# Performance work log

Hardware: AMD Instinct MI355X
Metric: run time of the kernel (lower is better)

## Reference

```python
import jax, jax.numpy as jnp
import numpy as np

# SamplesLoss('sinkhorn', p=2, blur=0.05, backend='tensorized') defaults (geomloss):
# debiased Sinkhorn divergence, cost C(x,y)=|x-y|^2/2, eps = blur^p,
# epsilon-scaling from diameter^p down to blur^p with scaling=0.5,
# symmetric (averaged) log-domain updates + one final extrapolation step.
P = 2
BLUR = 0.05
SCALING = 0.5
DIAMETER = 10.0  # static diameter estimate for the annealing schedule (randn data)


def _eps_schedule():
    eps_target = BLUR ** P
    lst = []
    e = DIAMETER ** P
    while e > eps_target:
        lst.append(e)
        e *= SCALING ** P
    lst.append(eps_target)
    return lst

EPS_LIST = _eps_schedule()


def _sqcost(x, y):
    # C[b,n,m] = 0.5 * ||x_bn - y_bm||^2, via expansion (avoids [B,N,M,D] tensor)
    x2 = jnp.sum(x * x, axis=-1)  # [B,N]
    y2 = jnp.sum(y * y, axis=-1)  # [B,M]
    xy = jnp.einsum('bnd,bmd->bnm', x, y)
    return 0.5 * (x2[:, :, None] + y2[:, None, :] - 2.0 * xy)


def _softmin(eps, C, h):
    # h: [B,M] (already log-weights + potential/eps); C: [B,N,M] -> [B,N]
    return -eps * jax.nn.logsumexp(h[:, None, :] - C / eps, axis=2)


def _sinkhorn_divergence(x, y, a, b):
    log_a = jnp.log(a)
    log_b = jnp.log(b)
    Cxy = _sqcost(x, y)
    Cyx = jnp.swapaxes(Cxy, 1, 2)
    Cxx = _sqcost(x, x)
    Cyy = _sqcost(y, y)

    eps0 = EPS_LIST[0]
    f_ba = _softmin(eps0, Cxy, log_b)  # potential on x for OT(a,b)
    g_ab = _softmin(eps0, Cyx, log_a)  # potential on y for OT(a,b)
    f_aa = _softmin(eps0, Cxx, log_a)  # debias self-potential on x
    g_bb = _softmin(eps0, Cyy, log_b)  # debias self-potential on y

    for eps in EPS_LIST:
        ft = _softmin(eps, Cxy, log_b + g_ab / eps)
        gt = _softmin(eps, Cyx, log_a + f_ba / eps)
        f_ba = 0.5 * (f_ba + ft)
        g_ab = 0.5 * (g_ab + gt)
        f_aa = 0.5 * (f_aa + _softmin(eps, Cxx, log_a + f_aa / eps))
        g_bb = 0.5 * (g_bb + _softmin(eps, Cyy, log_b + g_bb / eps))

    # final (non-averaged) extrapolation at the target temperature
    eps = EPS_LIST[-1]
    f_fin = _softmin(eps, Cxy, log_b + g_ab / eps)
    g_fin = _softmin(eps, Cyx, log_a + f_ba / eps)
    f_aa = _softmin(eps, Cxx, log_a + f_aa / eps)
    g_bb = _softmin(eps, Cyy, log_b + g_bb / eps)

    # debiased divergence: <a, f_ab - f_aa> + <b, g_ab - g_bb>
    return jnp.sum(a * (f_fin - f_aa), axis=-1) + jnp.sum(b * (g_fin - g_bb), axis=-1)


def setup_inputs() -> dict:
    key = jax.random.key(0)
    k1, k2, k3, k4 = jax.random.split(key, 4)
    B, N, M, D = 8, 2048, 2048, 64
    return {
        'inp1': jax.random.normal(k1, (B, N, D), dtype=jnp.float32),
        'inp2': jax.random.normal(k2, (B, M, D), dtype=jnp.float32),
        'weights1': jax.random.uniform(k3, (B, N), dtype=jnp.float32),
        'weights2': jax.random.uniform(k4, (B, M), dtype=jnp.float32),
    }


def reference(inp1, inp2, weights1, weights2):
    # normalize_weights=True branch of SinkhornLoss.forward
    mass1 = jnp.sum(weights1, axis=1, keepdims=True)
    mass1 = jnp.where(mass1 == 0.0, 1.0, mass1)
    a = weights1 / mass1
    mass2 = jnp.sum(weights2, axis=1, keepdims=True)
    mass2 = jnp.where(mass2 == 0.0, 1.0, mass2)
    b = weights2 / mass2
    loss = _sinkhorn_divergence(inp1, inp2, a, b)  # [B]
    return jnp.mean(loss)  # reduction='mean'
```

## Files before the change

### kernel.cpp

```cpp
#include <hip/hip_runtime.h>
#include <cstdint>
#include <cstddef>

#define BB 8
#define NPTS 2048
#define DIM 64
#define CK 64
#define NC (NPTS / CK)
#define BROWS 64

typedef _Float16 f16x8 __attribute__((ext_vector_type(8)));
typedef float f32x4 __attribute__((ext_vector_type(4)));

static const float EPS_H[9] = {100.0f, 25.0f, 6.25f, 1.5625f, 0.390625f,
                               0.09765625f, 0.0244140625f, 0.006103515625f,
                               0.0025f};

#if __has_builtin(__builtin_amdgcn_exp2f)
static __device__ __forceinline__ float fexp2(float x) {
  return __builtin_amdgcn_exp2f(x);
}
#else
static __device__ __forceinline__ float fexp2(float x) {
  float r;
  asm("v_exp_f32 %0, %1" : "=v"(r) : "v"(x));
  return r;
}
#endif

static __device__ __forceinline__ f32x4 vmax4(f32x4 a, f32x4 b) {
  f32x4 r;
  #pragma unroll
  for (int i = 0; i < 4; ++i) r[i] = fmaxf(a[i], b[i]);
  return r;
}

static __device__ __forceinline__ f32x4 vexp2_4(f32x4 a) {
  f32x4 r;
  #pragma unroll
  for (int i = 0; i < 4; ++i) r[i] = fexp2(a[i]);
  return r;
}

static __device__ __forceinline__ void gload_lds16(const void* g, void* l) {
  __builtin_amdgcn_global_load_lds(
      (const __attribute__((address_space(1))) void*)g,
      (__attribute__((address_space(3))) void*)l, 16, 0, 0);
}

struct SMTask {
  const _Float16* P;
  const _Float16* Q;
  const float* logw;
  const float* pot;
  const float* qsq;
  const float* psq;
  const float* oldf;
  float* out;
};


__global__ __launch_bounds__(256) void norm_weights_k(
    const float* __restrict__ w, float* __restrict__ aout,
    float* __restrict__ logout, int n) {
  int b = blockIdx.x;
  const float* wb = w + (size_t)b * n;
  __shared__ float red[256];
  float s = 0.f;
  for (int i = threadIdx.x; i < n; i += 256) s += wb[i];
  red[threadIdx.x] = s;
  __syncthreads();
  for (int st = 128; st > 0; st >>= 1) {
    if (threadIdx.x < st) red[threadIdx.x] += red[threadIdx.x + st];
    __syncthreads();
  }
  float mass = red[0];
  if (mass == 0.f) mass = 1.f;
  float inv = 1.f / mass;
  for (int i = threadIdx.x; i < n; i += 256) {
    float av = wb[i] * inv;
    aout[(size_t)b * n + i] = av;
    logout[(size_t)b * n + i] = logf(av);
  }
}

__global__ __launch_bounds__(256) void sqnorm_cvt_k(
    const float* __restrict__ X, float* __restrict__ sq,
    _Float16* __restrict__ Xh, int rows) {
  int row = blockIdx.x * 4 + (threadIdx.x >> 6);
  int lane = threadIdx.x & 63;
  if (row >= rows) return;
  float v = X[(size_t)row * DIM + lane];
  Xh[(size_t)row * DIM + lane] = (_Float16)v;
  float s = v * v;
  #pragma unroll
  for (int off = 32; off > 0; off >>= 1) s += __shfl_xor(s, off);
  if (lane == 0) sq[row] = s;
}

__global__ __launch_bounds__(256, 4) void fused_softmin_k(
    SMTask t0, SMTask t1, SMTask t2, SMTask t3, float ie2, float neg_eps_ln2) {
  __shared__ float hq[NPTS];
  __shared__ __align__(16) _Float16 qb[2][CK * DIM];
  SMTask T = (blockIdx.z == 0) ? t0
           : (blockIdx.z == 1) ? t1
           : (blockIdx.z == 2) ? t2 : t3;
  const int b = blockIdx.y;
  const int tid = threadIdx.x;
  const float LOG2E = 1.4426950408889634f;
  {
    const float* lw = T.logw + (size_t)b * NPTS;
    const float* q2 = T.qsq + (size_t)b * NPTS;
    const float* pt = T.pot ? T.pot + (size_t)b * NPTS : nullptr;
    for (int m = tid; m < NPTS; m += 256) {
      float h = fmaf(lw[m], LOG2E, -0.5f * q2[m] * ie2);
      if (pt) h = fmaf(pt[m], ie2, h);
      hq[m] = h;
    }
  }

  const int lane = tid & 63, wave = tid >> 6;
  const _Float16* Qb = T.Q + (size_t)b * NPTS * DIM;

  auto stage = [&](int buf, int chunk) {
    int m0 = chunk * CK;
    #pragma unroll
    for (int r = 0; r < 2; ++r) {
      int gbase = r * 256 + wave * 64;
      int gid = gbase + lane;
      int row = gid >> 3;
      int kg = (gid & 7) ^ (row & 7);
      const _Float16* src = Qb + (size_t)(m0 + row) * DIM + kg * 8;
      _Float16* dst = &qb[buf][(size_t)gbase * 8];
      gload_lds16(src, dst);
    }
  };

  const int fr = lane & 15;
  const int g0 = lane >> 4;
  const int r0 = blockIdx.x * BROWS + wave * 16;
  const _Float16* Pb = T.P + ((size_t)b * NPTS + r0) * DIM;
  f16x8 a0 = *(const f16x8*)(Pb + fr * DIM + g0 * 8);
  f16x8 a1 = *(const f16x8*)(Pb + fr * DIM + g0 * 8 + 32);

  f32x4 mx4 = {-3.0e38f, -3.0e38f, -3.0e38f, -3.0e38f};
  f32x4 sm4 = {0.f, 0.f, 0.f, 0.f};

  auto compute = [&](int cur, int m0) {
    const char* qbase = (const char*)&qb[cur][0];
    f32x4 v4[4];
    f32x4 cmx = mx4;
    #pragma unroll
    for (int s = 0; s < 4; ++s) {
      int row = s * 16 + fr;
      int byte0 = row * 128 + ((g0 ^ (row & 7)) << 4);
      int byte1 = row * 128 + (((g0 + 4) ^ (row & 7)) << 4);
      f16x8 b0 = *(const f16x8*)(qbase + byte0);
      f16x8 b1 = *(const f16x8*)(qbase + byte1);
      float hs = hq[m0 + s * 16 + fr];
      f32x4 z = {0.f, 0.f, 0.f, 0.f};
      f32x4 t = __builtin_amdgcn_mfma_f32_16x16x32_f16(a0, b0, z, 0, 0, 0);
      f32x4 acc = __builtin_amdgcn_mfma_f32_16x16x32_f16(a1, b1, t, 0, 0, 0);
      v4[s] = acc * ie2 + hs;
      cmx = vmax4(cmx, v4[s]);
    }
    f32x4 resc = vexp2_4(mx4 - cmx);
    f32x4 esum = vexp2_4(v4[0] - cmx) + vexp2_4(v4[1] - cmx);
    esum += vexp2_4(v4[2] - cmx) + vexp2_4(v4[3] - cmx);
    sm4 = sm4 * resc + esum;
    mx4 = cmx;
  };

  stage(0, 0);
  __syncthreads();

  for (int c = 0; c < NC - 1; ++c) {
    int cur = c & 1;
    stage(cur ^ 1, c + 1);
    asm volatile("s_waitcnt vmcnt(2)" ::: "memory");
    __builtin_amdgcn_sched_barrier(0);
    __builtin_amdgcn_s_barrier();
    __builtin_amdgcn_sched_barrier(0);
    compute(cur, c * CK);
    __builtin_amdgcn_sched_barrier(0);
    __builtin_amdgcn_s_barrier();
    __builtin_amdgcn_sched_barrier(0);
  }
  asm volatile("s_waitcnt vmcnt(0)" ::: "memory");
  __builtin_amdgcn_sched_barrier(0);
  __builtin_amdgcn_s_barrier();
  __builtin_amdgcn_sched_barrier(0);
  compute((NC - 1) & 1, (NC - 1) * CK);

  #pragma unroll
  for (int off = 1; off < 16; off <<= 1) {
    #pragma unroll
    for (int q = 0; q < 4; ++q) {
      float omx = __shfl_xor(mx4[q], off);
      float osm = __shfl_xor(sm4[q], off);
      float nm = fmaxf(mx4[q], omx);
      sm4[q] = sm4[q] * fexp2(mx4[q] - nm) + osm * fexp2(omx - nm);
      mx4[q] = nm;
    }
  }
  if (fr == 0) {
    #pragma unroll
    for (int q = 0; q < 4; ++q) {
      int r = r0 + g0 * 4 + q;
      size_t oi = (size_t)b * NPTS + r;
      float f = neg_eps_ln2 * (__log2f(sm4[q]) + mx4[q]) + 0.5f * T.psq[oi];
      if (T.oldf) f = 0.5f * (T.oldf[oi] + f);
      T.out[oi] = f;
    }
  }
}

__global__ __launch_bounds__(256) void loss_part_k(
    const float* __restrict__ aW, const float* __restrict__ f_fin,
    const float* __restrict__ f_aa, const float* __restrict__ bW,
    const float* __restrict__ g_fin, const float* __restrict__ g_bb,
    float* __restrict__ part) {
  __shared__ float red[256];
  int i0 = blockIdx.x * 256 + threadIdx.x;
  float s = 0.f;
  for (int i = i0; i < BB * NPTS; i += 64 * 256)
    s += aW[i] * (f_fin[i] - f_aa[i]) + bW[i] * (g_fin[i] - g_bb[i]);
  red[threadIdx.x] = s;
  __syncthreads();
  for (int st = 128; st > 0; st >>= 1) {
    if (threadIdx.x < st) red[threadIdx.x] += red[threadIdx.x + st];
    __syncthreads();
  }
  if (threadIdx.x == 0) part[blockIdx.x] = red[0];
}

__global__ __launch_bounds__(64) void loss_fin_k(const float* __restrict__ part,
                                                 float* __restrict__ out) {
  float s = part[threadIdx.x];
  #pragma unroll
  for (int off = 32; off > 0; off >>= 1) s += __shfl_xor(s, off);
  if (threadIdx.x == 0) out[0] = s * (1.f / BB);
}

__global__ void write_val_k(float* out, float v) { out[0] = v; }


extern "C" void kernel_launch(void* const* d_in, const int* in_sizes, int n_in,
                              void* d_out, int out_size, void* d_ws,
                              size_t ws_size, hipStream_t stream) {
  (void)in_sizes; (void)n_in; (void)out_size;
  const float* X = (const float*)d_in[0];
  const float* Y = (const float*)d_in[1];
  const float* W1 = (const float*)d_in[2];
  const float* W2 = (const float*)d_in[3];
  float* out = (float*)d_out;

  char* base = (char*)d_ws;
  size_t off = 0;
  auto alloc_b = [&](size_t bytes) {
    void* r = base + off;
    off += (bytes + 255) & ~(size_t)255;
    return r;
  };
  const size_t nP = (size_t)BB * NPTS;
  _Float16* Xh = (_Float16*)alloc_b(nP * DIM * 2);
  _Float16* Yh = (_Float16*)alloc_b(nP * DIM * 2);
  float* x2 = (float*)alloc_b(nP * 4);
  float* y2 = (float*)alloc_b(nP * 4);
  float* aW = (float*)alloc_b(nP * 4);
  float* bW = (float*)alloc_b(nP * 4);
  float* la = (float*)alloc_b(nP * 4);
  float* lb = (float*)alloc_b(nP * 4);
  float* fba[2] = {(float*)alloc_b(nP * 4), (float*)alloc_b(nP * 4)};
  float* gab[2] = {(float*)alloc_b(nP * 4), (float*)alloc_b(nP * 4)};
  float* faa[2] = {(float*)alloc_b(nP * 4), (float*)alloc_b(nP * 4)};
  float* gbb[2] = {(float*)alloc_b(nP * 4), (float*)alloc_b(nP * 4)};
  float* part = (float*)alloc_b(64 * 4);
  if (ws_size < off) {
    write_val_k<<<1, 1, 0, stream>>>(out, -(float)(ws_size >> 20));
    return;
  }

  norm_weights_k<<<BB, 256, 0, stream>>>(W1, aW, la, NPTS);
  norm_weights_k<<<BB, 256, 0, stream>>>(W2, bW, lb, NPTS);
  sqnorm_cvt_k<<<BB * NPTS / 4, 256, 0, stream>>>(X, x2, Xh, BB * NPTS);
  sqnorm_cvt_k<<<BB * NPTS / 4, 256, 0, stream>>>(Y, y2, Yh, BB * NPTS);

  const float LN2 = 0.6931471805599453f;
  const float LOG2E = 1.4426950408889634f;
  dim3 fg(NPTS / BROWS, BB, 4);

  auto launch4 = [&](SMTask A, SMTask B2, SMTask C, SMTask D2, float eps) {
    float ie2 = LOG2E / eps;
    float nel = -eps * LN2;
    fused_softmin_k<<<fg, 256, 0, stream>>>(A, B2, C, D2, ie2, nel);
  };

  {
    float e = EPS_H[0];
    launch4(
        SMTask{Xh, Yh, lb, nullptr, y2, x2, nullptr, fba[0]},
        SMTask{Yh, Xh, la, nullptr, x2, y2, nullptr, gab[0]},
        SMTask{Xh, Xh, la, nullptr, x2, x2, nullptr, faa[0]},
        SMTask{Yh, Yh, lb, nullptr, y2, y2, nullptr, gbb[0]},
        e);
  }

  int cur = 0;
  for (int it = 0; it < 9; ++it) {
    float e = EPS_H[it];
    int nxt = cur ^ 1;
    launch4(
        SMTask{Xh, Yh, lb, gab[cur], y2, x2, fba[cur], fba[nxt]},
        SMTask{Yh, Xh, la, fba[cur], x2, y2, gab[cur], gab[nxt]},
        SMTask{Xh, Xh, la, faa[cur], x2, x2, faa[cur], faa[nxt]},
        SMTask{Yh, Yh, lb, gbb[cur], y2, y2, gbb[cur], gbb[nxt]},
        e);
    cur = nxt;
  }

  {
    float e = EPS_H[8];
    int nxt = cur ^ 1;
    launch4(
        SMTask{Xh, Yh, lb, gab[cur], y2, x2, nullptr, fba[nxt]},
        SMTask{Yh, Xh, la, fba[cur], x2, y2, nullptr, gab[nxt]},
        SMTask{Xh, Xh, la, faa[cur], x2, x2, nullptr, faa[nxt]},
        SMTask{Yh, Yh, lb, gbb[cur], y2, y2, nullptr, gbb[nxt]},
        e);
    loss_part_k<<<64, 256, 0, stream>>>(aW, fba[nxt], faa[nxt], bW, gab[nxt],
                                        gbb[nxt], part);
    loss_fin_k<<<1, 64, 0, stream>>>(part, out);
  }
}
```

Measured before the change: 502.6 us.

## Split softmin reduction over two column halves with a separate merge kernel

Each softmin block now covers only half of the column range (a split-K over the logsumexp), which doubles the grid to 2048 blocks and raises the occupancy hint to 8. Partial max and sum values are written to global memory and combined by a new merge kernel. That kernel also precomputes the next iteration's h vector into a global buffer, so the per-block h setup becomes a plain copy. The aim is better GPU fill and less redundant per-block setup, at the cost of an extra launch per iteration and extra global traffic for the partials.

```diff
diff --git a/kernel.cpp b/kernel.cpp
--- a/kernel.cpp
+++ b/kernel.cpp
@@ -6,7 +6,8 @@
 #define NPTS 2048
 #define DIM 64
 #define CK 64
-#define NC (NPTS / CK)
+#define HALFC 1024
+#define NC (HALFC / CK)
 #define BROWS 64
 
 typedef _Float16 f16x8 __attribute__((ext_vector_type(8)));
@@ -15,6 +16,8 @@
 static const float EPS_H[9] = {100.0f, 25.0f, 6.25f, 1.5625f, 0.390625f,
                                0.09765625f, 0.0244140625f, 0.006103515625f,
                                0.0025f};
+#define LOG2E 1.4426950408889634f
+#define LN2 0.6931471805599453f
 
 #if __has_builtin(__builtin_amdgcn_exp2f)
 static __device__ __forceinline__ float fexp2(float x) {
@@ -48,15 +51,17 @@
       (__attribute__((address_space(3))) void*)l, 16, 0, 0);
 }
 
-struct SMTask {
+struct FT {
   const _Float16* P;
   const _Float16* Q;
-  const float* logw;
-  const float* pot;
-  const float* qsq;
+};
+struct MT {
   const float* psq;
   const float* oldf;
   float* out;
+  const float* lwn;
+  const float* q2n;
+  float* hqn;
 };
 
 
@@ -98,29 +103,39 @@
   if (lane == 0) sq[row] = s;
 }
 
-__global__ __launch_bounds__(256, 4) void fused_softmin_k(
-    SMTask t0, SMTask t1, SMTask t2, SMTask t3, float ie2, float neg_eps_ln2) {
-  __shared__ float hq[NPTS];
+__global__ __launch_bounds__(256) void init_hq_k(
+    const float* __restrict__ la, const float* __restrict__ lb,
+    const float* __restrict__ x2, const float* __restrict__ y2,
+    float* __restrict__ hq, float ie2) {
+  int task = blockIdx.z;
+  int idx = blockIdx.x * 256 + threadIdx.x;
+  const float* lw = (task == 1 || task == 2) ? la : lb;
+  const float* q2 = (task == 1 || task == 2) ? x2 : y2;
+  hq[(size_t)task * BB * NPTS + idx] =
+      fmaf(lw[idx], LOG2E, -0.5f * q2[idx] * ie2);
+}
+
+__global__ __launch_bounds__(256, 8) void fused_softmin_k(
+    FT t0, FT t1, FT t2, FT t3, const float* __restrict__ hqG,
+    float* __restrict__ pmx, float* __restrict__ psm, float ie2) {
+  __shared__ float hql[HALFC];
   __shared__ __align__(16) _Float16 qb[2][CK * DIM];
-  SMTask T = (blockIdx.z == 0) ? t0
-           : (blockIdx.z == 1) ? t1
-           : (blockIdx.z == 2) ? t2 : t3;
-  const int b = blockIdx.y;
+  FT T = (blockIdx.z == 0) ? t0
+       : (blockIdx.z == 1) ? t1
+       : (blockIdx.z == 2) ? t2 : t3;
+  const int rowg = blockIdx.x >> 1, half = blockIdx.x & 1;
+  const int b = blockIdx.y, task = blockIdx.z;
   const int tid = threadIdx.x;
-  const float LOG2E = 1.4426950408889634f;
+
   {
-    const float* lw = T.logw + (size_t)b * NPTS;
-    const float* q2 = T.qsq + (size_t)b * NPTS;
-    const float* pt = T.pot ? T.pot + (size_t)b * NPTS : nullptr;
-    for (int m = tid; m < NPTS; m += 256) {
-      float h = fmaf(lw[m], LOG2E, -0.5f * q2[m] * ie2);
-      if (pt) h = fmaf(pt[m], ie2, h);
-      hq[m] = h;
-    }
+    const float* hqp = hqG + ((size_t)task * BB + b) * NPTS + half * HALFC;
+    #pragma unroll
+    for (int i = 0; i < HALFC / 256; ++i)
+      hql[i * 256 + tid] = hqp[i * 256 + tid];
   }
 
   const int lane = tid & 63, wave = tid >> 6;
-  const _Float16* Qb = T.Q + (size_t)b * NPTS * DIM;
+  const _Float16* Qb = T.Q + ((size_t)b * NPTS + half * HALFC) * DIM;
 
   auto stage = [&](int buf, int chunk) {
     int m0 = chunk * CK;
@@ -138,7 +153,7 @@
 
   const int fr = lane & 15;
   const int g0 = lane >> 4;
-  const int r0 = blockIdx.x * BROWS + wave * 16;
+  const int r0 = rowg * BROWS + wave * 16;
   const _Float16* Pb = T.P + ((size_t)b * NPTS + r0) * DIM;
   f16x8 a0 = *(const f16x8*)(Pb + fr * DIM + g0 * 8);
   f16x8 a1 = *(const f16x8*)(Pb + fr * DIM + g0 * 8 + 32);
@@ -157,7 +172,7 @@
       int byte1 = row * 128 + (((g0 + 4) ^ (row & 7)) << 4);
       f16x8 b0 = *(const f16x8*)(qbase + byte0);
       f16x8 b1 = *(const f16x8*)(qbase + byte1);
-      float hs = hq[m0 + s * 16 + fr];
+      float hs = hql[m0 + s * 16 + fr];
       f32x4 z = {0.f, 0.f, 0.f, 0.f};
       f32x4 t = __builtin_amdgcn_mfma_f32_16x16x32_f16(a0, b0, z, 0, 0, 0);
       f32x4 acc = __builtin_amdgcn_mfma_f32_16x16x32_f16(a1, b1, t, 0, 0, 0);
@@ -207,11 +222,32 @@
     #pragma unroll
     for (int q = 0; q < 4; ++q) {
       int r = r0 + g0 * 4 + q;
-      size_t oi = (size_t)b * NPTS + r;
-      float f = neg_eps_ln2 * (__log2f(sm4[q]) + mx4[q]) + 0.5f * T.psq[oi];
-      if (T.oldf) f = 0.5f * (T.oldf[oi] + f);
-      T.out[oi] = f;
+      size_t pi = (((size_t)task * BB + b) * 2 + half) * NPTS + r;
+      pmx[pi] = mx4[q];
+      psm[pi] = sm4[q];
     }
+  }
+}
+
+__global__ __launch_bounds__(256) void merge_k(
+    const float* __restrict__ pmx, const float* __restrict__ psm,
+    MT m0, MT m1, MT m2, MT m3, float nel, float ie2n, int whq) {
+  int task = blockIdx.z;
+  MT M = (task == 0) ? m0 : (task == 1) ? m1 : (task == 2) ? m2 : m3;
+  int idx = blockIdx.x * 256 + threadIdx.x;
+  int b = idx >> 11;
+  int r = idx & 2047;
+  size_t pi = (((size_t)task * BB + b) * 2) * NPTS + r;
+  float ma = pmx[pi], mb = pmx[pi + NPTS];
+  float sa = psm[pi], sb = psm[pi + NPTS];
+  float nm = fmaxf(ma, mb);
+  float ss = sa * fexp2(ma - nm) + sb * fexp2(mb - nm);
+  float f = nel * (__log2f(ss) + nm) + 0.5f * M.psq[idx];
+  if (M.oldf) f = 0.5f * (M.oldf[idx] + f);
+  M.out[idx] = f;
+  if (whq) {
+    float h = fmaf(f, ie2n, fmaf(M.lwn[idx], LOG2E, -0.5f * M.q2n[idx] * ie2n));
+    M.hqn[idx] = h;
   }
 }
 
@@ -275,6 +311,9 @@
   float* gab[2] = {(float*)alloc_b(nP * 4), (float*)alloc_b(nP * 4)};
   float* faa[2] = {(float*)alloc_b(nP * 4), (float*)alloc_b(nP * 4)};
   float* gbb[2] = {(float*)alloc_b(nP * 4), (float*)alloc_b(nP * 4)};
+  float* hq = (float*)alloc_b(4 * nP * 4);
+  float* pmx = (float*)alloc_b(4 * nP * 2 * 4);
+  float* psm = (float*)alloc_b(4 * nP * 2 * 4);
   float* part = (float*)alloc_b(64 * 4);
   if (ws_size < off) {
     write_val_k<<<1, 1, 0, stream>>>(out, -(float)(ws_size >> 20));
@@ -286,48 +325,51 @@
   sqnorm_cvt_k<<<BB * NPTS / 4, 256, 0, stream>>>(X, x2, Xh, BB * NPTS);
   sqnorm_cvt_k<<<BB * NPTS / 4, 256, 0, stream>>>(Y, y2, Yh, BB * NPTS);
 
-  const float LN2 = 0.6931471805599453f;
-  const float LOG2E = 1.4426950408889634f;
-  dim3 fg(NPTS / BROWS, BB, 4);
-
-  auto launch4 = [&](SMTask A, SMTask B2, SMTask C, SMTask D2, float eps) {
-    float ie2 = LOG2E / eps;
+  dim3 fg(64, BB, 4);
+  dim3 mg(BB * NPTS / 256, 1, 4);
+
+  FT t0{Xh, Yh}, t1{Yh, Xh}, t2{Xh, Xh}, t3{Yh, Yh};
+  float* hq0 = hq;
+  float* hq1 = hq + 1 * nP;
+  float* hq2 = hq + 2 * nP;
+  float* hq3 = hq + 3 * nP;
+
+  auto fused = [&](float eps) {
+    fused_softmin_k<<<fg, 256, 0, stream>>>(t0, t1, t2, t3, hq, pmx, psm,
+                                            LOG2E / eps);
+  };
+  auto merge = [&](float eps, float ie2n, int whq, const float* oF,
+                   float* nF, const float* oG, float* nG, const float* oA,
+                   float* nA, const float* oB, float* nB) {
     float nel = -eps * LN2;
-    fused_softmin_k<<<fg, 256, 0, stream>>>(A, B2, C, D2, ie2, nel);
-  };
-
-  {
-    float e = EPS_H[0];
-    launch4(
-        SMTask{Xh, Yh, lb, nullptr, y2, x2, nullptr, fba[0]},
-        SMTask{Yh, Xh, la, nullptr, x2, y2, nullptr, gab[0]},
-        SMTask{Xh, Xh, la, nullptr, x2, x2, nullptr, faa[0]},
-        SMTask{Yh, Yh, lb, nullptr, y2, y2, nullptr, gbb[0]},
-        e);
-  }
+    MT M0{x2, oF, nF, la, x2, hq1};
+    MT M1{y2, oG, nG, lb, y2, hq0};
+    MT M2{x2, oA, nA, la, x2, hq2};
+    MT M3{y2, oB, nB, lb, y2, hq3};
+    merge_k<<<mg, 256, 0, stream>>>(pmx, psm, M0, M1, M2, M3, nel, ie2n, whq);
+  };
+
+  init_hq_k<<<mg, 256, 0, stream>>>(la, lb, x2, y2, hq, LOG2E / EPS_H[0]);
+
+  fused(EPS_H[0]);
+  merge(EPS_H[0], LOG2E / EPS_H[0], 1, nullptr, fba[0], nullptr, gab[0],
+        nullptr, faa[0], nullptr, gbb[0]);
 
   int cur = 0;
   for (int it = 0; it < 9; ++it) {
-    float e = EPS_H[it];
     int nxt = cur ^ 1;
-    launch4(
-        SMTask{Xh, Yh, lb, gab[cur], y2, x2, fba[cur], fba[nxt]},
-        SMTask{Yh, Xh, la, fba[cur], x2, y2, gab[cur], gab[nxt]},
-        SMTask{Xh, Xh, la, faa[cur], x2, x2, faa[cur], faa[nxt]},
-        SMTask{Yh, Yh, lb, gbb[cur], y2, y2, gbb[cur], gbb[nxt]},
-        e);
+    float epsn = EPS_H[it < 8 ? it + 1 : 8];
+    fused(EPS_H[it]);
+    merge(EPS_H[it], LOG2E / epsn, 1, fba[cur], fba[nxt], gab[cur], gab[nxt],
+          faa[cur], faa[nxt], gbb[cur], gbb[nxt]);
     cur = nxt;
   }
 
   {
-    float e = EPS_H[8];
     int nxt = cur ^ 1;
-    launch4(
-        SMTask{Xh, Yh, lb, gab[cur], y2, x2, nullptr, fba[nxt]},
-        SMTask{Yh, Xh, la, fba[cur], x2, y2, nullptr, gab[nxt]},
-        SMTask{Xh, Xh, la, faa[cur], x2, x2, nullptr, faa[nxt]},
-        SMTask{Yh, Yh, lb, gbb[cur], y2, y2, nullptr, gbb[nxt]},
-        e);
+    fused(EPS_H[8]);
+    merge(EPS_H[8], 0.f, 0, nullptr, fba[nxt], nullptr, gab[nxt], nullptr,
+          faa[nxt], nullptr, gbb[nxt]);
     loss_part_k<<<64, 256, 0, stream>>>(aW, fba[nxt], faa[nxt], bW, gab[nxt],
                                         gbb[nxt], part);
     loss_fin_k<<<1, 64, 0, stream>>>(part, out);
```

Result: faster. 466.7 us (-7.2%).
